# Performance work log

Hardware: AMD Instinct MI355X
Metric: run time of the kernel (lower is better)

The kernel has to match this reference:

```python
import jax, jax.numpy as jnp
import numpy as np

NUM_PIDS = 5532
NUM_CQ = 5000
D = 256
N = 8192
OIM_SCALAR = 30.0
IGNORE = 5554  # hardcoded ignore_index in the original F.cross_entropy call


def _l2norm(x):
    return x / jnp.linalg.norm(x, axis=-1, keepdims=True)


def setup_inputs() -> dict:
    key = jax.random.key(0)
    k0, k1, k2, k3, k4, k5 = jax.random.split(key, 6)
    inputs = _l2norm(jax.random.normal(k0, (N, D), dtype=jnp.float32))
    label = jax.random.randint(k1, (N,), 0, NUM_PIDS)
    label = jnp.where(jax.random.uniform(k2, (N,)) < 0.1, IGNORE, label).astype(jnp.int64)
    ious = jax.random.uniform(k3, (N,), minval=0.5, maxval=1.0, dtype=jnp.float32)
    lut = _l2norm(jax.random.normal(k4, (NUM_PIDS, D), dtype=jnp.float32))
    cq = _l2norm(jax.random.normal(k5, (NUM_CQ, D), dtype=jnp.float32))
    reliability = 0.5 * jnp.ones((NUM_PIDS + NUM_CQ,), dtype=jnp.float32)
    return {"inputs": inputs, "label": label, "ious": ious,
            "lut": lut, "cq": cq, "reliability": reliability}


def reference(inputs, label, ious, lut, cq, reliability):
    # OIM.forward: logits = [inputs @ lut.T | inputs @ cq.T] * reliability, then * oim_scalar
    bank = jnp.concatenate([lut, cq], axis=0)              # [num_pids+num_cq, D]
    logits = (inputs @ bank.T) * reliability[None, :] * OIM_SCALAR  # [N, L]
    # F.cross_entropy(projected, label, ignore_index=5554): mean over non-ignored rows
    logp = jax.nn.log_softmax(logits, axis=-1)
    valid = label != IGNORE
    safe = jnp.where(valid, label, 0)
    nll = -jnp.take_along_axis(logp, safe[:, None], axis=1)[:, 0]
    n_valid = jnp.maximum(jnp.sum(valid.astype(jnp.float32)), 1.0)
    loss = jnp.sum(jnp.where(valid, nll, 0.0)) / n_valid
    return loss
```

## Files before the change

kernel.cpp:

```cpp
#include <hip/hip_runtime.h>
#include <stdint.h>

#define NROWS 8192
#define DDIM 256
#define NPIDS 5532
#define NCQ 5000
#define LCOLS 10532
#define IGNORE_IDX 5554
#define NT 83
#define LPAD (NT * 128)
#define NSPLIT 8
#define NPARTS (NSPLIT * 2)
#define PADCOLS (LPAD - LCOLS)
#define TSTEP (NSPLIT * 65536)
#define OIM_SCALE 30.0f
#define LOG2E 1.4426950408889634f
#define LN2f 0.6931471805599453f

using f32x4 = __attribute__((ext_vector_type(4))) float;
using bf16x8 = __attribute__((ext_vector_type(8))) __bf16;
using ushort8 = __attribute__((ext_vector_type(8))) unsigned short;

#define WS_INBF 0u
#define WS_BANK 4194304u
#define WS_PARTS 9633792u
#define WS_RLOGIT 10158080u
#define WS_BLK 10190848u
#define WS_NEED 10191104u

__device__ __forceinline__ unsigned short f2bf(float f) {
  union { float f; uint32_t u; } v; v.f = f;
  uint32_t u = v.u;
  uint32_t r = (u + 0x7FFFu + ((u >> 16) & 1u)) >> 16;
  return (unsigned short)r;
}

__device__ __forceinline__ void async16(const void* g, void* l) {
  __builtin_amdgcn_global_load_lds(
      (const __attribute__((address_space(1))) uint32_t*)g,
      (__attribute__((address_space(3))) uint32_t*)l, 16, 0, 0);
}

__global__ void prep_kernel(const float* __restrict__ inputs,
                            const float* __restrict__ lut,
                            const float* __restrict__ cq,
                            const float* __restrict__ rel,
                            unsigned short* __restrict__ in2,
                            unsigned short* __restrict__ bank3) {
  const int GIN = NROWS * (DDIM / 8);
  const int GBK = LPAD * (DDIM / 8);
  const int total = GIN + GBK;
  for (int d = blockIdx.x * blockDim.x + threadIdx.x; d < total;
       d += gridDim.x * blockDim.x) {
    const float* src = nullptr;
    unsigned short* dst;
    float scale = 1.0f;
    bool zero = false;
    if (d < GIN) {
      const int R = ((d >> 9) << 4) | (d & 15);
      const int c8 = (((d >> 6) & 7) << 2) | ((d >> 4) & 3);
      src = inputs + R * DDIM + c8 * 8;
      dst = in2 + (size_t)d * 8;
    } else {
      const int b = d - GIN;
      const int R = ((b >> 12) << 7) | (((b >> 9) & 7) << 4) | (b & 15);
      const int c8 = (((b >> 6) & 7) << 2) | ((b >> 4) & 3);
      dst = bank3 + (size_t)b * 8;
      if (R < NPIDS) src = lut + (size_t)R * DDIM + c8 * 8;
      else if (R < LCOLS) src = cq + (size_t)(R - NPIDS) * DDIM + c8 * 8;
      else zero = true;
      if (!zero) scale = OIM_SCALE * LOG2E * rel[R];
    }
    ushort8 o = {0, 0, 0, 0, 0, 0, 0, 0};
    if (!zero) {
      const f32x4* s4 = (const f32x4*)src;
      f32x4 v0 = s4[0], v1 = s4[1];
      o[0] = f2bf(v0[0] * scale); o[1] = f2bf(v0[1] * scale);
      o[2] = f2bf(v0[2] * scale); o[3] = f2bf(v0[3] * scale);
      o[4] = f2bf(v1[0] * scale); o[5] = f2bf(v1[1] * scale);
      o[6] = f2bf(v1[2] * scale); o[7] = f2bf(v1[3] * scale);
    }
    *(ushort8*)dst = o;
  }
}

#define STG(PP)                                                           \
  do {                                                                    \
    char* _d = dT + (((PP) + 2) & 3) * 16384;                             \
    async16(sgP, _d);                                                     \
    async16(sgP + 32768, _d + 8192);                                      \
    sgP += ((PP) == 1) ? (TSTEP - 6144) : 2048;                           \
  } while (0)

#define PHASE(PP, VMN)                                                    \
  do {                                                                    \
    asm volatile("s_waitcnt vmcnt(" #VMN ")" ::: "memory");               \
    asm volatile("s_barrier" ::: "memory");                               \
    const char* _c = rB + (PP) * 16384;                                   \
    bf16x8 bF[4][2];                                                      \
    _Pragma("unroll") for (int _ni = 0; _ni < 4; ++_ni)                   \
      _Pragma("unroll") for (int _kl = 0; _kl < 2; ++_kl)                 \
        bF[_ni][_kl] = *(const bf16x8*)(_c + _ni * 2048 + _kl * 1024);    \
    asm volatile("s_waitcnt lgkmcnt(0)" ::: "memory");                    \
    __builtin_amdgcn_sched_barrier(0);                                    \
    __builtin_amdgcn_s_setprio(1);                                        \
    _Pragma("unroll") for (int _kl = 0; _kl < 2; ++_kl)                   \
      _Pragma("unroll") for (int _mi = 0; _mi < 4; ++_mi)                 \
        _Pragma("unroll") for (int _ni = 0; _ni < 4; ++_ni)               \
          acc[_mi][_ni] = __builtin_amdgcn_mfma_f32_16x16x32_bf16(        \
              aR[_mi][(PP) * 2 + _kl], bF[_ni][_kl],                      \
              ((PP) == 0 && _kl == 0) ? vzero : acc[_mi][_ni], 0, 0, 0);  \
    __builtin_amdgcn_s_setprio(0);                                        \
  } while (0)

__global__ __launch_bounds__(512, 2) void oim_main_kernel(
    const unsigned short* __restrict__ in2,
    const unsigned short* __restrict__ bank3,
    float* __restrict__ parts) {
  extern __shared__ char ring[];
  const int tid = threadIdx.x;
  const int lane = tid & 63;
  const int wv = tid >> 6;
  const int wrow = wv >> 1;
  const int wcol = wv & 1;
  const int ql = lane & 15;
  const int h = lane >> 4;

  const int bid = blockIdx.x;
  const int sp = bid & 7;
  const int bm = bid >> 3;
  const int ntiles = (sp < 3) ? 11 : 10;

  bf16x8 aR[4][8];
  {
    const char* ab =
        (const char*)in2 + (size_t)(bm * 16 + wrow * 4) * 8192 + lane * 16;
#pragma unroll
    for (int mi = 0; mi < 4; ++mi)
#pragma unroll
      for (int kk = 0; kk < 8; ++kk)
        aR[mi][kk] = *(const bf16x8*)(ab + mi * 8192 + kk * 1024);
  }
  const int rowb = bm * 256 + wrow * 64 + h * 4;

  asm volatile("" ::: "memory");

  const char* sgT = (const char*)bank3 + (size_t)sp * 65536 +
                    (tid >> 7) * 8192 + (tid & 127) * 16;
  char* dT = ring + tid * 16;

  async16(sgT, dT);
  async16(sgT + 32768, dT + 8192);
  asm volatile("" ::: "memory");
  async16(sgT + 2048, dT + 16384);
  async16(sgT + 2048 + 32768, dT + 16384 + 8192);
  asm volatile("" ::: "memory");
  const char* sgP = sgT + 4096;

  const char* rB = ring + (wcol * 4) * 2048 + lane * 16;

  const f32x4 vzero = {0.f, 0.f, 0.f, 0.f};
  f32x4 acc[4][4];
  float se[4][4];
#pragma unroll
  for (int a = 0; a < 4; ++a)
#pragma unroll
    for (int b = 0; b < 4; ++b) se[a][b] = 0.f;

  for (int t = 0; t < ntiles - 1; ++t) {
    STG(0); PHASE(0, 4);
    STG(1); PHASE(1, 4);
    STG(2); PHASE(2, 4);
    STG(3); PHASE(3, 4);
#pragma unroll
    for (int mi = 0; mi < 4; ++mi)
#pragma unroll
      for (int ni = 0; ni < 4; ++ni)
#pragma unroll
        for (int r = 0; r < 4; ++r)
          se[mi][r] += __builtin_amdgcn_exp2f(acc[mi][ni][r]);
  }
  STG(0); PHASE(0, 4);
  STG(1); PHASE(1, 4);
  PHASE(2, 2);
  PHASE(3, 0);
#pragma unroll
  for (int mi = 0; mi < 4; ++mi)
#pragma unroll
    for (int ni = 0; ni < 4; ++ni)
#pragma unroll
      for (int r = 0; r < 4; ++r)
        se[mi][r] += __builtin_amdgcn_exp2f(acc[mi][ni][r]);

#pragma unroll
  for (int mi = 0; mi < 4; ++mi)
#pragma unroll
    for (int r = 0; r < 4; ++r) {
      float v = se[mi][r];
      v += __shfl_xor(v, 1);
      v += __shfl_xor(v, 2);
      v += __shfl_xor(v, 4);
      v += __shfl_xor(v, 8);
      se[mi][r] = v;
    }
  if (ql == 0) {
    const int part = sp * 2 + wcol;
#pragma unroll
    for (int mi = 0; mi < 4; ++mi) {
      f32x4 o = {se[mi][0], se[mi][1], se[mi][2], se[mi][3]};
      *(f32x4*)(parts + (size_t)part * NROWS + rowb + mi * 16) = o;
    }
  }
}

__global__ void label_logit_kernel(const float* __restrict__ inputs,
                                   const int* __restrict__ label,
                                   const float* __restrict__ lut,
                                   const float* __restrict__ cq,
                                   const float* __restrict__ rel,
                                   float* __restrict__ rowlogit) {
  const int lane = threadIdx.x & 63;
  const int wv = threadIdx.x >> 6;
  const int row = blockIdx.x * 4 + wv;
  if (row >= NROWS) return;
  const int l = label[row];
  float out = 0.0f;
  if (l != IGNORE_IDX && l >= 0 && l < LCOLS) {
    const float* bk = (l < NPIDS) ? (lut + (size_t)l * DDIM)
                                  : (cq + (size_t)(l - NPIDS) * DDIM);
    f32x4 a = *(const f32x4*)(inputs + (size_t)row * DDIM + lane * 4);
    f32x4 b = *(const f32x4*)(bk + lane * 4);
    float d = a[0] * b[0] + a[1] * b[1] + a[2] * b[2] + a[3] * b[3];
#pragma unroll
    for (int m = 1; m < 64; m <<= 1) d += __shfl_xor(d, m);
    out = OIM_SCALE * rel[l] * d;
  }
  if (lane == 0) rowlogit[row] = out;
}

__global__ void reduce1_kernel(const float* __restrict__ parts,
                               const float* __restrict__ rowlogit,
                               const int* __restrict__ label,
                               float* __restrict__ blk) {
  const int r = blockIdx.x * 256 + threadIdx.x;
  float s = 0.0f, c = 0.0f;
  if (label[r] != IGNORE_IDX) {
    float tot = 0.0f;
#pragma unroll
    for (int p = 0; p < NPARTS; ++p) tot += parts[p * NROWS + r];
    tot -= (float)PADCOLS;
    s = LN2f * __builtin_log2f(tot) - rowlogit[r];
    c = 1.0f;
  }
#pragma unroll
  for (int m = 1; m < 64; m <<= 1) {
    s += __shfl_xor(s, m);
    c += __shfl_xor(c, m);
  }
  __shared__ float ss[4], sc[4];
  const int wv = threadIdx.x >> 6, lane = threadIdx.x & 63;
  if (lane == 0) { ss[wv] = s; sc[wv] = c; }
  __syncthreads();
  if (threadIdx.x == 0) {
    blk[blockIdx.x * 2 + 0] = ss[0] + ss[1] + ss[2] + ss[3];
    blk[blockIdx.x * 2 + 1] = sc[0] + sc[1] + sc[2] + sc[3];
  }
}

__global__ void reduce2_kernel(const float* __restrict__ blk,
                               float* __restrict__ out) {
  const int lane = threadIdx.x;
  float s = (lane < 32) ? blk[lane * 2 + 0] : 0.0f;
  float c = (lane < 32) ? blk[lane * 2 + 1] : 0.0f;
#pragma unroll
  for (int m = 1; m < 32; m <<= 1) {
    s += __shfl_xor(s, m);
    c += __shfl_xor(c, m);
  }
  if (lane == 0) out[0] = s / fmaxf(c, 1.0f);
}

extern "C" void kernel_launch(void* const* d_in, const int* in_sizes, int n_in,
                              void* d_out, int out_size, void* d_ws,
                              size_t ws_size, hipStream_t stream) {
  const float* inputs = (const float*)d_in[0];
  const int* label = (const int*)d_in[1];
  const float* lut = (const float*)d_in[3];
  const float* cq = (const float*)d_in[4];
  const float* rel = (const float*)d_in[5];
  float* out = (float*)d_out;
  char* ws = (char*)d_ws;
  if (ws_size < WS_NEED) return;

  unsigned short* in2 = (unsigned short*)(ws + WS_INBF);
  unsigned short* bank3 = (unsigned short*)(ws + WS_BANK);
  float* parts = (float*)(ws + WS_PARTS);
  float* rowlogit = (float*)(ws + WS_RLOGIT);
  float* blk = (float*)(ws + WS_BLK);

  hipFuncSetAttribute((const void*)oim_main_kernel,
                      hipFuncAttributeMaxDynamicSharedMemorySize, 65536);

  prep_kernel<<<dim3(1024), dim3(256), 0, stream>>>(inputs, lut, cq, rel,
                                                    in2, bank3);
  label_logit_kernel<<<dim3(2048), dim3(256), 0, stream>>>(inputs, label, lut,
                                                           cq, rel, rowlogit);
  oim_main_kernel<<<dim3(256), dim3(512), 65536, stream>>>(in2, bank3, parts);
  reduce1_kernel<<<dim3(32), dim3(256), 0, stream>>>(parts, rowlogit, label,
                                                     blk);
  reduce2_kernel<<<dim3(1), dim3(64), 0, stream>>>(blk, out);
}
```

Before: 60.73 us.

## Deepen LDS ring to five stages and double-buffer B fragments with interleaved exp

The main GEMM kernel's shared-memory ring grows from four to five 16KB slots, with three stages prefetched up front. LDS reads for the next phase are issued into a second register bank (ping-pong bA/bB) before the current phase's MFMAs run, so reads overlap compute. The exp2 accumulation of finished tiles is folded into the last MFMA cluster. The cost is more LDS (80KB) and more registers, and launch bounds drop to one block per SM, which may lower occupancy on a 256-block grid.

```diff
diff --git a/kernel.cpp b/kernel.cpp
--- a/kernel.cpp
+++ b/kernel.cpp
@@ -84,36 +84,71 @@
   }
 }
 
-#define STG(PP)                                                           \
-  do {                                                                    \
-    char* _d = dT + (((PP) + 2) & 3) * 16384;                             \
+#define STG()                                                             \
+  do {                                                                    \
+    char* _d = ring + roS + tid * 16;                                     \
     async16(sgP, _d);                                                     \
     async16(sgP + 32768, _d + 8192);                                      \
-    sgP += ((PP) == 1) ? (TSTEP - 6144) : 2048;                           \
-  } while (0)
-
-#define PHASE(PP, VMN)                                                    \
-  do {                                                                    \
-    asm volatile("s_waitcnt vmcnt(" #VMN ")" ::: "memory");               \
-    asm volatile("s_barrier" ::: "memory");                               \
-    const char* _c = rB + (PP) * 16384;                                   \
-    bf16x8 bF[4][2];                                                      \
-    _Pragma("unroll") for (int _ni = 0; _ni < 4; ++_ni)                   \
-      _Pragma("unroll") for (int _kl = 0; _kl < 2; ++_kl)                 \
-        bF[_ni][_kl] = *(const bf16x8*)(_c + _ni * 2048 + _kl * 1024);    \
-    asm volatile("s_waitcnt lgkmcnt(0)" ::: "memory");                    \
-    __builtin_amdgcn_sched_barrier(0);                                    \
-    __builtin_amdgcn_s_setprio(1);                                        \
+    roS += 16384; if (roS == 81920) roS = 0;                              \
+  } while (0)
+
+#define DSREAD8(BANK, RO)                                                 \
+  do {                                                                    \
+    const char* _p = rB + (RO);                                           \
+    _Pragma("unroll") for (int _f = 0; _f < 8; ++_f)                      \
+      BANK[_f] =                                                          \
+          *(const bf16x8*)(_p + (_f >> 1) * 2048 + (_f & 1) * 1024);      \
+  } while (0)
+
+#define CLUSTERN(PP, BC)                                                  \
+  do {                                                                    \
     _Pragma("unroll") for (int _kl = 0; _kl < 2; ++_kl)                   \
       _Pragma("unroll") for (int _mi = 0; _mi < 4; ++_mi)                 \
         _Pragma("unroll") for (int _ni = 0; _ni < 4; ++_ni)               \
           acc[_mi][_ni] = __builtin_amdgcn_mfma_f32_16x16x32_bf16(        \
-              aR[_mi][(PP) * 2 + _kl], bF[_ni][_kl],                      \
+              aR[_mi][(PP) * 2 + _kl], BC[_ni * 2 + _kl],                 \
               ((PP) == 0 && _kl == 0) ? vzero : acc[_mi][_ni], 0, 0, 0);  \
+  } while (0)
+
+#define CLUSTER3(BC)                                                      \
+  do {                                                                    \
+    _Pragma("unroll") for (int _mi = 0; _mi < 4; ++_mi)                   \
+      _Pragma("unroll") for (int _ni = 0; _ni < 4; ++_ni)                 \
+        acc[_mi][_ni] = __builtin_amdgcn_mfma_f32_16x16x32_bf16(          \
+            aR[_mi][6], BC[_ni * 2], acc[_mi][_ni], 0, 0, 0);             \
+    _Pragma("unroll") for (int _i = 0; _i < 16; ++_i) {                   \
+      const int _mi = _i >> 2, _ni = _i & 3;                              \
+      acc[_mi][_ni] = __builtin_amdgcn_mfma_f32_16x16x32_bf16(            \
+          aR[_mi][7], BC[_ni * 2 + 1], acc[_mi][_ni], 0, 0, 0);           \
+      if (_i >= 3) {                                                      \
+        const int _pm = (_i - 3) >> 2, _pn = (_i - 3) & 3;                \
+        _Pragma("unroll") for (int _r = 0; _r < 4; ++_r)                  \
+          se[_pm][_r] += __builtin_amdgcn_exp2f(acc[_pm][_pn][_r]);       \
+      }                                                                   \
+    }                                                                     \
+    _Pragma("unroll") for (int _p = 13; _p < 16; ++_p) {                  \
+      const int _pm = _p >> 2, _pn = _p & 3;                              \
+      _Pragma("unroll") for (int _r = 0; _r < 4; ++_r)                    \
+        se[_pm][_r] += __builtin_amdgcn_exp2f(acc[_pm][_pn][_r]);         \
+    }                                                                     \
+  } while (0)
+
+#define PHN(PP, BC, BN)                                                   \
+  do {                                                                    \
+    asm volatile("s_waitcnt vmcnt(2)" ::: "memory");                      \
+    asm volatile("s_barrier" ::: "memory");                               \
+    STG();                                                                \
+    sgP += ((PP) == 0) ? (TSTEP - 6144) : 2048;                           \
+    DSREAD8(BN, roN);                                                     \
+    roN += 16384; if (roN == 81920) roN = 0;                              \
+    asm volatile("s_waitcnt lgkmcnt(8)" ::: "memory");                    \
+    __builtin_amdgcn_sched_barrier(0);                                    \
+    __builtin_amdgcn_s_setprio(1);                                        \
+    if ((PP) == 3) { CLUSTER3(BC); } else { CLUSTERN(PP, BC); }           \
     __builtin_amdgcn_s_setprio(0);                                        \
   } while (0)
 
-__global__ __launch_bounds__(512, 2) void oim_main_kernel(
+__global__ __launch_bounds__(512, 1) void oim_main_kernel(
     const unsigned short* __restrict__ in2,
     const unsigned short* __restrict__ bank3,
     float* __restrict__ parts) {
@@ -147,17 +182,17 @@
 
   const char* sgT = (const char*)bank3 + (size_t)sp * 65536 +
                     (tid >> 7) * 8192 + (tid & 127) * 16;
-  char* dT = ring + tid * 16;
-
-  async16(sgT, dT);
-  async16(sgT + 32768, dT + 8192);
-  asm volatile("" ::: "memory");
-  async16(sgT + 2048, dT + 16384);
-  async16(sgT + 2048 + 32768, dT + 16384 + 8192);
-  asm volatile("" ::: "memory");
-  const char* sgP = sgT + 4096;
-
-  const char* rB = ring + (wcol * 4) * 2048 + lane * 16;
+#pragma unroll
+  for (int p = 0; p < 3; ++p) {
+    char* d = ring + p * 16384 + tid * 16;
+    async16(sgT + p * 2048, d);
+    async16(sgT + p * 2048 + 32768, d + 8192);
+  }
+  const char* sgP = sgT + 6144;
+  int roS = 49152;
+  int roN = 16384;
+
+  const char* rB = ring + wcol * 8192 + lane * 16;
 
   const f32x4 vzero = {0.f, 0.f, 0.f, 0.f};
   f32x4 acc[4][4];
@@ -167,30 +202,40 @@
 #pragma unroll
     for (int b = 0; b < 4; ++b) se[a][b] = 0.f;
 
+  asm volatile("s_waitcnt vmcnt(4)" ::: "memory");
+  asm volatile("s_barrier" ::: "memory");
+  bf16x8 bA[8], bB[8];
+  DSREAD8(bA, 0);
+
   for (int t = 0; t < ntiles - 1; ++t) {
-    STG(0); PHASE(0, 4);
-    STG(1); PHASE(1, 4);
-    STG(2); PHASE(2, 4);
-    STG(3); PHASE(3, 4);
-#pragma unroll
-    for (int mi = 0; mi < 4; ++mi)
-#pragma unroll
-      for (int ni = 0; ni < 4; ++ni)
-#pragma unroll
-        for (int r = 0; r < 4; ++r)
-          se[mi][r] += __builtin_amdgcn_exp2f(acc[mi][ni][r]);
-  }
-  STG(0); PHASE(0, 4);
-  STG(1); PHASE(1, 4);
-  PHASE(2, 2);
-  PHASE(3, 0);
-#pragma unroll
-  for (int mi = 0; mi < 4; ++mi)
-#pragma unroll
-    for (int ni = 0; ni < 4; ++ni)
-#pragma unroll
-      for (int r = 0; r < 4; ++r)
-        se[mi][r] += __builtin_amdgcn_exp2f(acc[mi][ni][r]);
+    PHN(0, bA, bB);
+    PHN(1, bB, bA);
+    PHN(2, bA, bB);
+    PHN(3, bB, bA);
+  }
+  PHN(0, bA, bB);
+  asm volatile("s_waitcnt vmcnt(2)" ::: "memory");
+  asm volatile("s_barrier" ::: "memory");
+  DSREAD8(bA, roN);
+  roN += 16384; if (roN == 81920) roN = 0;
+  asm volatile("s_waitcnt lgkmcnt(8)" ::: "memory");
+  __builtin_amdgcn_sched_barrier(0);
+  __builtin_amdgcn_s_setprio(1);
+  CLUSTERN(1, bB);
+  __builtin_amdgcn_s_setprio(0);
+  asm volatile("s_waitcnt vmcnt(0)" ::: "memory");
+  asm volatile("s_barrier" ::: "memory");
+  DSREAD8(bB, roN);
+  asm volatile("s_waitcnt lgkmcnt(8)" ::: "memory");
+  __builtin_amdgcn_sched_barrier(0);
+  __builtin_amdgcn_s_setprio(1);
+  CLUSTERN(2, bA);
+  __builtin_amdgcn_s_setprio(0);
+  asm volatile("s_waitcnt lgkmcnt(0)" ::: "memory");
+  __builtin_amdgcn_sched_barrier(0);
+  __builtin_amdgcn_s_setprio(1);
+  CLUSTER3(bB);
+  __builtin_amdgcn_s_setprio(0);
 
 #pragma unroll
   for (int mi = 0; mi < 4; ++mi)
@@ -299,13 +344,13 @@
   float* blk = (float*)(ws + WS_BLK);
 
   hipFuncSetAttribute((const void*)oim_main_kernel,
-                      hipFuncAttributeMaxDynamicSharedMemorySize, 65536);
+                      hipFuncAttributeMaxDynamicSharedMemorySize, 81920);
 
   prep_kernel<<<dim3(1024), dim3(256), 0, stream>>>(inputs, lut, cq, rel,
                                                     in2, bank3);
   label_logit_kernel<<<dim3(2048), dim3(256), 0, stream>>>(inputs, label, lut,
                                                            cq, rel, rowlogit);
-  oim_main_kernel<<<dim3(256), dim3(512), 65536, stream>>>(in2, bank3, parts);
+  oim_main_kernel<<<dim3(256), dim3(512), 81920, stream>>>(in2, bank3, parts);
   reduce1_kernel<<<dim3(32), dim3(256), 0, stream>>>(parts, rowlogit, label,
                                                      blk);
   reduce2_kernel<<<dim3(1), dim3(64), 0, stream>>>(blk, out);
```

After: 73.18 us. +20.5%, slower.

## Deepen LDS ring to six stages with paired barriers and split-k LDS loads

Applied to the files above, without the earlier changes.

Grows the shared-memory staging ring from four to six 16KB slots and issues two stage loads per barrier, cutting barriers per tile from four to two. Each compute phase splits its B-fragment LDS reads into two halves so the first MFMA group can start while the second half is still loading. Launch bounds drop from two blocks per CU to one because of the larger 96KB LDS footprint. The deeper prefetch is meant to hide global-load latency, but the kernel now runs at lower occupancy, and the grid of 256 blocks may map unevenly to the CUs.

```diff
diff --git a/kernel.cpp b/kernel.cpp
--- a/kernel.cpp
+++ b/kernel.cpp
@@ -84,36 +84,51 @@
   }
 }
 
-#define STG(PP)                                                           \
+#define STGS()                                                            \
   do {                                                                    \
-    char* _d = dT + (((PP) + 2) & 3) * 16384;                             \
-    async16(sgP, _d);                                                     \
-    async16(sgP + 32768, _d + 8192);                                      \
-    sgP += ((PP) == 1) ? (TSTEP - 6144) : 2048;                           \
+    if (S < NQ) {                                                         \
+      char* _d = ring + roS + tid * 16;                                   \
+      async16(sgP, _d);                                                   \
+      async16(sgP + 32768, _d + 8192);                                    \
+      sgP += ((S & 3) == 3) ? (TSTEP - 6144) : 2048;                      \
+      roS += 16384; if (roS == 98304) roS = 0;                            \
+      ++S;                                                                \
+    }                                                                     \
   } while (0)
 
-#define PHASE(PP, VMN)                                                    \
+#define COMP(PP)                                                          \
+  do {                                                                    \
+    const char* _c = rB + roN;                                            \
+    bf16x8 b0[4], b1[4];                                                  \
+    _Pragma("unroll") for (int _ni = 0; _ni < 4; ++_ni)                   \
+      b0[_ni] = *(const bf16x8*)(_c + _ni * 2048);                        \
+    _Pragma("unroll") for (int _ni = 0; _ni < 4; ++_ni)                   \
+      b1[_ni] = *(const bf16x8*)(_c + _ni * 2048 + 1024);                 \
+    asm volatile("s_waitcnt lgkmcnt(4)" ::: "memory");                    \
+    __builtin_amdgcn_sched_barrier(0);                                    \
+    __builtin_amdgcn_s_setprio(1);                                        \
+    _Pragma("unroll") for (int _mi = 0; _mi < 4; ++_mi)                   \
+      _Pragma("unroll") for (int _ni = 0; _ni < 4; ++_ni)                 \
+        acc[_mi][_ni] = __builtin_amdgcn_mfma_f32_16x16x32_bf16(          \
+            aR[_mi][(PP) * 2], b0[_ni],                                   \
+            ((PP) == 0) ? vzero : acc[_mi][_ni], 0, 0, 0);                \
+    asm volatile("s_waitcnt lgkmcnt(0)" ::: "memory");                    \
+    __builtin_amdgcn_sched_barrier(0);                                    \
+    _Pragma("unroll") for (int _mi = 0; _mi < 4; ++_mi)                   \
+      _Pragma("unroll") for (int _ni = 0; _ni < 4; ++_ni)                 \
+        acc[_mi][_ni] = __builtin_amdgcn_mfma_f32_16x16x32_bf16(          \
+            aR[_mi][(PP) * 2 + 1], b1[_ni], acc[_mi][_ni], 0, 0, 0);      \
+    __builtin_amdgcn_s_setprio(0);                                        \
+    roN += 16384; if (roN == 98304) roN = 0;                              \
+  } while (0)
+
+#define VMB(VMN)                                                          \
   do {                                                                    \
     asm volatile("s_waitcnt vmcnt(" #VMN ")" ::: "memory");               \
     asm volatile("s_barrier" ::: "memory");                               \
-    const char* _c = rB + (PP) * 16384;                                   \
-    bf16x8 bF[4][2];                                                      \
-    _Pragma("unroll") for (int _ni = 0; _ni < 4; ++_ni)                   \
-      _Pragma("unroll") for (int _kl = 0; _kl < 2; ++_kl)                 \
-        bF[_ni][_kl] = *(const bf16x8*)(_c + _ni * 2048 + _kl * 1024);    \
-    asm volatile("s_waitcnt lgkmcnt(0)" ::: "memory");                    \
-    __builtin_amdgcn_sched_barrier(0);                                    \
-    __builtin_amdgcn_s_setprio(1);                                        \
-    _Pragma("unroll") for (int _kl = 0; _kl < 2; ++_kl)                   \
-      _Pragma("unroll") for (int _mi = 0; _mi < 4; ++_mi)                 \
-        _Pragma("unroll") for (int _ni = 0; _ni < 4; ++_ni)               \
-          acc[_mi][_ni] = __builtin_amdgcn_mfma_f32_16x16x32_bf16(        \
-              aR[_mi][(PP) * 2 + _kl], bF[_ni][_kl],                      \
-              ((PP) == 0 && _kl == 0) ? vzero : acc[_mi][_ni], 0, 0, 0);  \
-    __builtin_amdgcn_s_setprio(0);                                        \
   } while (0)
 
-__global__ __launch_bounds__(512, 2) void oim_main_kernel(
+__global__ __launch_bounds__(512, 1) void oim_main_kernel(
     const unsigned short* __restrict__ in2,
     const unsigned short* __restrict__ bank3,
     float* __restrict__ parts) {
@@ -130,6 +145,7 @@
   const int sp = bid & 7;
   const int bm = bid >> 3;
   const int ntiles = (sp < 3) ? 11 : 10;
+  const int NQ = ntiles * 4;
 
   bf16x8 aR[4][8];
   {
@@ -147,17 +163,18 @@
 
   const char* sgT = (const char*)bank3 + (size_t)sp * 65536 +
                     (tid >> 7) * 8192 + (tid & 127) * 16;
-  char* dT = ring + tid * 16;
-
-  async16(sgT, dT);
-  async16(sgT + 32768, dT + 8192);
-  asm volatile("" ::: "memory");
-  async16(sgT + 2048, dT + 16384);
-  async16(sgT + 2048 + 32768, dT + 16384 + 8192);
-  asm volatile("" ::: "memory");
-  const char* sgP = sgT + 4096;
-
-  const char* rB = ring + (wcol * 4) * 2048 + lane * 16;
+#pragma unroll
+  for (int p = 0; p < 4; ++p) {
+    char* d = ring + p * 16384 + tid * 16;
+    async16(sgT + p * 2048, d);
+    async16(sgT + p * 2048 + 32768, d + 8192);
+  }
+  const char* sgP = sgT + TSTEP;
+  int S = 4;
+  int roS = 65536;
+  int roN = 0;
+
+  const char* rB = ring + wcol * 8192 + lane * 16;
 
   const f32x4 vzero = {0.f, 0.f, 0.f, 0.f};
   f32x4 acc[4][4];
@@ -168,10 +185,8 @@
     for (int b = 0; b < 4; ++b) se[a][b] = 0.f;
 
   for (int t = 0; t < ntiles - 1; ++t) {
-    STG(0); PHASE(0, 4);
-    STG(1); PHASE(1, 4);
-    STG(2); PHASE(2, 4);
-    STG(3); PHASE(3, 4);
+    VMB(4); STGS(); STGS(); COMP(0); COMP(1);
+    VMB(4); STGS(); STGS(); COMP(2); COMP(3);
 #pragma unroll
     for (int mi = 0; mi < 4; ++mi)
 #pragma unroll
@@ -180,10 +195,8 @@
         for (int r = 0; r < 4; ++r)
           se[mi][r] += __builtin_amdgcn_exp2f(acc[mi][ni][r]);
   }
-  STG(0); PHASE(0, 4);
-  STG(1); PHASE(1, 4);
-  PHASE(2, 2);
-  PHASE(3, 0);
+  VMB(4); COMP(0); COMP(1);
+  VMB(0); COMP(2); COMP(3);
 #pragma unroll
   for (int mi = 0; mi < 4; ++mi)
 #pragma unroll
@@ -299,13 +312,13 @@
   float* blk = (float*)(ws + WS_BLK);
 
   hipFuncSetAttribute((const void*)oim_main_kernel,
-                      hipFuncAttributeMaxDynamicSharedMemorySize, 65536);
+                      hipFuncAttributeMaxDynamicSharedMemorySize, 98304);
 
   prep_kernel<<<dim3(1024), dim3(256), 0, stream>>>(inputs, lut, cq, rel,
                                                     in2, bank3);
   label_logit_kernel<<<dim3(2048), dim3(256), 0, stream>>>(inputs, label, lut,
                                                            cq, rel, rowlogit);
-  oim_main_kernel<<<dim3(256), dim3(512), 65536, stream>>>(in2, bank3, parts);
+  oim_main_kernel<<<dim3(256), dim3(512), 98304, stream>>>(in2, bank3, parts);
   reduce1_kernel<<<dim3(32), dim3(256), 0, stream>>>(parts, rowlogit, label,
                                                      blk);
   reduce2_kernel<<<dim3(1), dim3(64), 0, stream>>>(blk, out);
```

Result: slower. 62.28 us (+2.5%).
